# Performance work log

Hardware: AMD Instinct MI355X
Metric: run time of the kernel (lower is better)

Reference implementation:

```python
import jax, jax.numpy as jnp
import numpy as np

TOP_K = 2
HEAD_NUM = 16


def setup_inputs() -> dict:
    key = jax.random.key(0)
    ks = jax.random.split(key, 6)
    B, H, N, D, G = 8, HEAD_NUM, 2048, 64, 128
    return {
        "q": jax.random.normal(ks[0], (B, H, N, D), dtype=jnp.float32),
        "k": jax.random.normal(ks[1], (B, H, N, D), dtype=jnp.float32),
        "v": jax.random.normal(ks[2], (B, H, N, D), dtype=jnp.float32),
        "gating_input": jax.random.normal(ks[3], (B, N, G), dtype=jnp.float32),
        "rank3_ninf_mask": jnp.zeros((B, N, N), dtype=jnp.float32),
        "W_gate": jax.random.normal(ks[4], (H, G), dtype=jnp.float32) * 0.02,
        "b_gate": jnp.zeros((H,), dtype=jnp.float32),
    }


def reference(q, k, v, gating_input, rank3_ninf_mask, W_gate, b_gate):
    B = q.shape[0]
    d = q.shape[-1]
    # --- router ---
    gate_logits = gating_input.mean(axis=1) @ W_gate.T + b_gate      # [B, H]
    gate_softmax = jax.nn.softmax(gate_logits, axis=1)               # [B, H]
    _, top_k_idx = jax.lax.top_k(gate_softmax, TOP_K)                # [B, K]
    gating_mask = jnp.zeros_like(gate_softmax).at[
        jnp.arange(B)[:, None], top_k_idx].set(1.0)
    # load balancing loss
    tokens_per_expert = gating_mask.sum(axis=0)                      # [H]
    density = tokens_per_expert / (tokens_per_expert.sum() + 1e-6)
    lb_loss = HEAD_NUM * jnp.sum(gate_softmax.mean(axis=0) * density)
    # --- gather selected heads: [B, K, N, D] ---
    idx = top_k_idx[:, :, None, None]
    q_sel = jnp.take_along_axis(q, idx, axis=1)
    k_sel = jnp.take_along_axis(k, idx, axis=1)
    v_sel = jnp.take_along_axis(v, idx, axis=1)
    # --- scaled dot attention ---
    score = jnp.einsum('bhqd,bhkd->bhqk', q_sel, k_sel) / jnp.sqrt(
        jnp.asarray(d, dtype=q.dtype))                               # [B,K,N,N]
    score = score + rank3_ninf_mask[:, None, :, :]
    weights = jax.nn.softmax(score, axis=3)
    out = jnp.einsum('bhqk,bhkd->bhqd', weights, v_sel)              # [B,K,N,D]
    B_, K_, N_, D_ = out.shape
    out = out.transpose(0, 2, 1, 3).reshape(B_, N_, K_ * D_)         # [B,N,K*D]
    return out, lb_loss
```

## Files before the change

kernel.cpp:

```cpp
#include <hip/hip_runtime.h>

#define NSEQ 2048
#define DH 64
#define NH 16
#define BQ 64
#define BKV 64
#define KP 72
#define VP 68
#define PART_STRIDE 4224

typedef __attribute__((ext_vector_type(8))) short bf16x8;
typedef __attribute__((ext_vector_type(4))) short s16x4;
typedef __attribute__((ext_vector_type(4))) float f32x4;

static __device__ __forceinline__ short f2bf(float f) {
    __bf16 b = (__bf16)f;
    return __builtin_bit_cast(short, b);
}

__global__ void gate_partial(const float* __restrict__ gi, float* __restrict__ wsA, int SL) {
    int b = blockIdx.x / SL, sl = blockIdx.x % SL;
    int rows = NSEQ / SL;
    int tid = threadIdx.x;
    int g = tid & 127, half = tid >> 7;
    float s = 0.f;
    int n0 = sl * rows;
    for (int n = n0 + half; n < n0 + rows; n += 2)
        s += gi[((size_t)b * NSEQ + n) * 128 + g];
    __shared__ float part[2][128];
    part[half][g] = s;
    __syncthreads();
    if (tid < 128) wsA[(b * SL + sl) * 128 + tid] = part[0][tid] + part[1][tid];
}

__global__ void gate_final(const float* __restrict__ wsA, const float* __restrict__ Wg,
                           const float* __restrict__ bg, float* __restrict__ ws_sm,
                           int* __restrict__ ws_idx, int SL) {
    int b = blockIdx.x, tid = threadIdx.x;
    __shared__ float meanv[128];
    __shared__ float logits[NH];
    if (tid < 128) {
        float s = 0.f;
        for (int sl = 0; sl < SL; ++sl) s += wsA[(b * SL + sl) * 128 + tid];
        meanv[tid] = s * (1.0f / NSEQ);
    }
    __syncthreads();
    if (tid < 128) {
        int h = tid >> 3, j = tid & 7;
        float p = 0.f;
        for (int i = 0; i < 16; ++i) { int g = j + 8 * i; p += meanv[g] * Wg[h * 128 + g]; }
        p += __shfl_xor(p, 1);
        p += __shfl_xor(p, 2);
        p += __shfl_xor(p, 4);
        if (j == 0) logits[h] = p + bg[h];
    }
    __syncthreads();
    if (tid == 0) {
        float mx = logits[0];
        for (int h = 1; h < NH; ++h) mx = fmaxf(mx, logits[h]);
        float e[NH], sum = 0.f;
        for (int h = 0; h < NH; ++h) { e[h] = __expf(logits[h] - mx); sum += e[h]; }
        float inv = 1.0f / sum;
        for (int h = 0; h < NH; ++h) ws_sm[b * NH + h] = e[h] * inv;
        int i1 = 0;
        for (int h = 1; h < NH; ++h) if (logits[h] > logits[i1]) i1 = h;
        int i2 = (i1 == 0) ? 1 : 0;
        for (int h = 0; h < NH; ++h) if (h != i1 && logits[h] > logits[i2]) i2 = h;
        ws_idx[b * 2 + 0] = i1;
        ws_idx[b * 2 + 1] = i2;
    }
}

__global__ void lb_kernel(const float* __restrict__ ws_sm, const int* __restrict__ ws_idx,
                          float* __restrict__ out_lb) {
    if (threadIdx.x == 0 && blockIdx.x == 0) {
        float counts[NH];
        for (int h = 0; h < NH; ++h) counts[h] = 0.f;
        for (int i = 0; i < 16; ++i) counts[ws_idx[i]] += 1.0f;
        float lb = 0.f;
        for (int h = 0; h < NH; ++h) {
            float msm = 0.f;
            for (int b = 0; b < 8; ++b) msm += ws_sm[b * NH + h];
            msm *= (1.0f / 8.0f);
            lb += msm * (counts[h] / (16.0f + 1e-6f));
        }
        out_lb[0] = lb * (float)NH;
    }
}

template<int SPLIT>
__global__ __launch_bounds__(256, 4)
void attn_kernel(const float* __restrict__ q, const float* __restrict__ k,
                 const float* __restrict__ v, const float* __restrict__ mask,
                 const int* __restrict__ topk, float* __restrict__ out,
                 float* __restrict__ part) {
    const int qt = blockIdx.x & 31;
    const int sp = blockIdx.x >> 5;
    const int kk = blockIdx.y;
    const int b  = blockIdx.z;
    const int h  = topk[b * 2 + kk];
    const int tid = threadIdx.x;
    const int wave = tid >> 6;
    const int lane = tid & 63;
    const int lr = lane & 15;
    const int lg = lane >> 4;

    const int nt = 32 / SPLIT;
    const int t_begin = sp * nt;

    __shared__ short Kb[BKV][KP];
    __shared__ short Vt[DH][VP];
    __shared__ short Pl[4][16][VP];

    const float QSC = 0.125f * 1.4426950408889634f;
    const float MSC = 1.4426950408889634f;

    const size_t headoff = ((size_t)b * NH + h) * (size_t)NSEQ * DH;

    bf16x8 qf[2];
    {
        const float* qp = q + headoff + (size_t)(qt * BQ + wave * 16 + lr) * DH;
        #pragma unroll
        for (int f = 0; f < 2; ++f) {
            const float* p = qp + f * 32 + lg * 8;
            float4 a = *(const float4*)p;
            float4 c = *(const float4*)(p + 4);
            qf[f][0] = f2bf(a.x * QSC); qf[f][1] = f2bf(a.y * QSC);
            qf[f][2] = f2bf(a.z * QSC); qf[f][3] = f2bf(a.w * QSC);
            qf[f][4] = f2bf(c.x * QSC); qf[f][5] = f2bf(c.y * QSC);
            qf[f][6] = f2bf(c.z * QSC); qf[f][7] = f2bf(c.w * QSC);
        }
    }

    f32x4 acc[4];
    float m_r[4], l_r[4];
    #pragma unroll
    for (int dt = 0; dt < 4; ++dt)
        for (int r = 0; r < 4; ++r) acc[dt][r] = 0.f;
    #pragma unroll
    for (int r = 0; r < 4; ++r) { m_r[r] = -INFINITY; l_r[r] = 0.f; }

    const float* kb = k + headoff;
    const float* vb = v + headoff;
    const float* mb = mask + (size_t)b * NSEQ * NSEQ + (size_t)(qt * BQ + wave * 16) * NSEQ;

    const int srow = tid >> 4;
    const int scol = (tid & 15) * 4;

    float4 kreg[4], vreg[4];
    float  mreg[16];

    auto issue_kv = [&](int t0) {
        #pragma unroll
        for (int pp = 0; pp < 4; ++pp) {
            int n = t0 + pp * 16 + srow;
            kreg[pp] = *(const float4*)(kb + (size_t)n * DH + scol);
            vreg[pp] = *(const float4*)(vb + (size_t)n * DH + scol);
        }
    };
    auto issue_mask = [&](int t0) {
        #pragma unroll
        for (int r = 0; r < 4; ++r) {
            const float* mp = mb + (size_t)(4 * lg + r) * NSEQ + t0 + lr;
            #pragma unroll
            for (int ct = 0; ct < 4; ++ct) mreg[r * 4 + ct] = mp[ct * 16];
        }
    };

    issue_kv(t_begin * BKV);
    issue_mask(t_begin * BKV);

    for (int t = 0; t < nt; ++t) {
        const int t0 = (t_begin + t) * BKV;
        __syncthreads();
        #pragma unroll
        for (int pp = 0; pp < 4; ++pp) {
            int n = pp * 16 + srow;
            s16x4 sk = { f2bf(kreg[pp].x), f2bf(kreg[pp].y), f2bf(kreg[pp].z), f2bf(kreg[pp].w) };
            *(s16x4*)&Kb[n][scol] = sk;
            Vt[scol + 0][n] = f2bf(vreg[pp].x);
            Vt[scol + 1][n] = f2bf(vreg[pp].y);
            Vt[scol + 2][n] = f2bf(vreg[pp].z);
            Vt[scol + 3][n] = f2bf(vreg[pp].w);
        }
        __syncthreads();

        f32x4 s[4];
        #pragma unroll
        for (int ct = 0; ct < 4; ++ct) {
            bf16x8 kf0 = *(const bf16x8*)&Kb[ct * 16 + lr][lg * 8];
            bf16x8 kf1 = *(const bf16x8*)&Kb[ct * 16 + lr][32 + lg * 8];
            f32x4 z; for (int r = 0; r < 4; ++r) z[r] = 0.f;
            z = __builtin_amdgcn_mfma_f32_16x16x32_bf16(qf[0], kf0, z, 0, 0, 0);
            z = __builtin_amdgcn_mfma_f32_16x16x32_bf16(qf[1], kf1, z, 0, 0, 0);
            s[ct] = z;
        }
        #pragma unroll
        for (int r = 0; r < 4; ++r)
            #pragma unroll
            for (int ct = 0; ct < 4; ++ct)
                s[ct][r] = fmaf(mreg[r * 4 + ct], MSC, s[ct][r]);

        if (t + 1 < nt) { issue_kv(t0 + BKV); issue_mask(t0 + BKV); }

        float mnew[4], sc[4], ps[4];
        #pragma unroll
        for (int r = 0; r < 4; ++r) {
            float tm = fmaxf(fmaxf(s[0][r], s[1][r]), fmaxf(s[2][r], s[3][r]));
            tm = fmaxf(tm, __shfl_xor(tm, 1));
            tm = fmaxf(tm, __shfl_xor(tm, 2));
            tm = fmaxf(tm, __shfl_xor(tm, 4));
            tm = fmaxf(tm, __shfl_xor(tm, 8));
            mnew[r] = fmaxf(m_r[r], tm);
            sc[r] = __builtin_amdgcn_exp2f(m_r[r] - mnew[r]);
            ps[r] = 0.f;
        }
        #pragma unroll
        for (int ct = 0; ct < 4; ++ct) {
            #pragma unroll
            for (int r = 0; r < 4; ++r) {
                float p = __builtin_amdgcn_exp2f(s[ct][r] - mnew[r]);
                ps[r] += p;
                Pl[wave][4 * lg + r][ct * 16 + lr] = f2bf(p);
            }
        }
        #pragma unroll
        for (int r = 0; r < 4; ++r) {
            float t2 = ps[r];
            t2 += __shfl_xor(t2, 1);
            t2 += __shfl_xor(t2, 2);
            t2 += __shfl_xor(t2, 4);
            t2 += __shfl_xor(t2, 8);
            l_r[r] = l_r[r] * sc[r] + t2;
            m_r[r] = mnew[r];
        }
        #pragma unroll
        for (int dt = 0; dt < 4; ++dt)
            for (int r = 0; r < 4; ++r) acc[dt][r] *= sc[r];

        s16x4 p00 = *(const s16x4*)&Pl[wave][lr][lg * 8];
        s16x4 p01 = *(const s16x4*)&Pl[wave][lr][lg * 8 + 4];
        s16x4 p10 = *(const s16x4*)&Pl[wave][lr][32 + lg * 8];
        s16x4 p11 = *(const s16x4*)&Pl[wave][lr][32 + lg * 8 + 4];
        bf16x8 pf0 = __builtin_shufflevector(p00, p01, 0, 1, 2, 3, 4, 5, 6, 7);
        bf16x8 pf1 = __builtin_shufflevector(p10, p11, 0, 1, 2, 3, 4, 5, 6, 7);
        #pragma unroll
        for (int dt = 0; dt < 4; ++dt) {
            s16x4 v00 = *(const s16x4*)&Vt[dt * 16 + lr][lg * 8];
            s16x4 v01 = *(const s16x4*)&Vt[dt * 16 + lr][lg * 8 + 4];
            s16x4 v10 = *(const s16x4*)&Vt[dt * 16 + lr][32 + lg * 8];
            s16x4 v11 = *(const s16x4*)&Vt[dt * 16 + lr][32 + lg * 8 + 4];
            bf16x8 vf0 = __builtin_shufflevector(v00, v01, 0, 1, 2, 3, 4, 5, 6, 7);
            bf16x8 vf1 = __builtin_shufflevector(v10, v11, 0, 1, 2, 3, 4, 5, 6, 7);
            acc[dt] = __builtin_amdgcn_mfma_f32_16x16x32_bf16(pf0, vf0, acc[dt], 0, 0, 0);
            acc[dt] = __builtin_amdgcn_mfma_f32_16x16x32_bf16(pf1, vf1, acc[dt], 0, 0, 0);
        }
    }

    if (SPLIT == 1) {
        #pragma unroll
        for (int r = 0; r < 4; ++r) {
            float inv = 1.0f / l_r[r];
            int qrow = qt * BQ + wave * 16 + 4 * lg + r;
            float* op = out + ((size_t)b * NSEQ + qrow) * 128 + kk * 64;
            for (int dt = 0; dt < 4; ++dt) op[dt * 16 + lr] = acc[dt][r] * inv;
        }
    } else {
        float* pp = part + (size_t)((((b * 2 + kk) * 32 + qt) * SPLIT) + sp) * PART_STRIDE;
        #pragma unroll
        for (int r = 0; r < 4; ++r) {
            int prow = wave * 16 + 4 * lg + r;
            float* op = pp + prow * 64;
            for (int dt = 0; dt < 4; ++dt) op[dt * 16 + lr] = acc[dt][r];
            if (lr == 0) {
                pp[4096 + prow] = m_r[r];
                pp[4160 + prow] = l_r[r];
            }
        }
    }
}

__global__ __launch_bounds__(256)
void combine_kernel(const float* __restrict__ part, float* __restrict__ out, int SPLIT) {
    const int qt = blockIdx.x, kk = blockIdx.y, b = blockIdx.z;
    const float* base = part + (size_t)(((b * 2 + kk) * 32 + qt) * SPLIT) * PART_STRIDE;
    const int row = threadIdx.x >> 2;
    const int c0 = (threadIdx.x & 3) << 4;

    float M = -INFINITY;
    for (int s = 0; s < SPLIT; ++s)
        M = fmaxf(M, base[(size_t)s * PART_STRIDE + 4096 + row]);

    float L = 0.f;
    float4 o[4];
    #pragma unroll
    for (int j = 0; j < 4; ++j) o[j] = make_float4(0.f, 0.f, 0.f, 0.f);

    for (int s = 0; s < SPLIT; ++s) {
        const float* pb = base + (size_t)s * PART_STRIDE;
        float w = exp2f(pb[4096 + row] - M);
        L += w * pb[4160 + row];
        const float4* ap = (const float4*)(pb + row * 64 + c0);
        #pragma unroll
        for (int j = 0; j < 4; ++j) {
            float4 a = ap[j];
            o[j].x += w * a.x; o[j].y += w * a.y;
            o[j].z += w * a.z; o[j].w += w * a.w;
        }
    }
    float inv = 1.0f / L;
    float* op = out + ((size_t)b * NSEQ + qt * 64 + row) * 128 + kk * 64 + c0;
    #pragma unroll
    for (int j = 0; j < 4; ++j) {
        float4 r = make_float4(o[j].x * inv, o[j].y * inv, o[j].z * inv, o[j].w * inv);
        ((float4*)op)[j] = r;
    }
}

extern "C" void kernel_launch(void* const* d_in, const int* in_sizes, int n_in,
                              void* d_out, int out_size, void* d_ws, size_t ws_size,
                              hipStream_t stream) {
    const float* q    = (const float*)d_in[0];
    const float* k    = (const float*)d_in[1];
    const float* v    = (const float*)d_in[2];
    const float* gi   = (const float*)d_in[3];
    const float* mask = (const float*)d_in[4];
    const float* Wg   = (const float*)d_in[5];
    const float* bg   = (const float*)d_in[6];
    float* out = (float*)d_out;

    const size_t part_bytes = (size_t)512 * 4 * PART_STRIDE * 4;
    const size_t needA = part_bytes + (size_t)8 * 64 * 128 * 4 + 4096;
    const size_t needB = 65536 + part_bytes;

    int SL, SPLIT;
    float* ws_part;
    float* wsA;
    if (ws_size >= needA) {
        SL = 64; SPLIT = 4;
        ws_part = (float*)d_ws;
        wsA = (float*)((char*)d_ws + part_bytes);
    } else if (ws_size >= needB) {
        SL = 8; SPLIT = 4;
        wsA = (float*)d_ws;
        ws_part = (float*)((char*)d_ws + 65536);
    } else {
        SL = 8; SPLIT = 1;
        wsA = (float*)d_ws;
        ws_part = (float*)d_ws;
    }
    float* ws_sm = wsA + 8 * SL * 128;
    int*   ws_idx = (int*)(ws_sm + 8 * NH);

    gate_partial<<<8 * SL, 256, 0, stream>>>(gi, wsA, SL);
    gate_final<<<8, 256, 0, stream>>>(wsA, Wg, bg, ws_sm, ws_idx, SL);
    lb_kernel<<<1, 64, 0, stream>>>(ws_sm, ws_idx, out + (size_t)8 * NSEQ * 128);

    dim3 grid(32 * SPLIT, 2, 8);
    if (SPLIT == 4) {
        attn_kernel<4><<<grid, 256, 0, stream>>>(q, k, v, mask, ws_idx, out, ws_part);
        dim3 cgrid(32, 2, 8);
        combine_kernel<<<cgrid, 256, 0, stream>>>(ws_part, out, SPLIT);
    } else {
        attn_kernel<1><<<grid, 256, 0, stream>>>(q, k, v, mask, ws_idx, out, ws_part);
    }
}
```

Before: 114.9 us.

## Switch attention to 32x32x16 MFMA with 128-row query tiles and lazy rescale

Rewrites the attention kernel to use 32x32x16 bf16 MFMA with transposed S=K·Q^T, so each wave covers 32 query rows and a block covers 128. P fragments are built in registers through cross-half lane shuffles instead of a round trip through shared memory. Running-max rescaling is skipped unless the max grows past a threshold. K/V staging uses wider LDS stores, and the load-balance scalar is folded into the combine kernel so one launch is removed. The trade-offs are fewer blocks in the grid, a lower occupancy hint, and the thresholded rescale, which lets exp2 arguments reach up to the threshold (2^10) before renormalising.

New measurement: 117.7 us. +2.5%, slower.

```diff
diff --git a/kernel.cpp b/kernel.cpp
--- a/kernel.cpp
+++ b/kernel.cpp
@@ -3,15 +3,14 @@
 #define NSEQ 2048
 #define DH 64
 #define NH 16
-#define BQ 64
 #define BKV 64
-#define KP 72
-#define VP 68
-#define PART_STRIDE 4224
+#define PSTRIDE 8448
 
 typedef __attribute__((ext_vector_type(8))) short bf16x8;
 typedef __attribute__((ext_vector_type(4))) short s16x4;
 typedef __attribute__((ext_vector_type(4))) float f32x4;
+typedef __attribute__((ext_vector_type(16))) float f32x16;
+typedef __attribute__((ext_vector_type(4))) unsigned u32x4;
 
 static __device__ __forceinline__ short f2bf(float f) {
     __bf16 b = (__bf16)f;
@@ -71,100 +70,122 @@
     }
 }
 
+static __device__ __forceinline__ void lb_compute(const float* ws_sm, const int* ws_idx,
+                                                  float* out_lb) {
+    float counts[NH];
+    for (int h = 0; h < NH; ++h) counts[h] = 0.f;
+    for (int i = 0; i < 16; ++i) counts[ws_idx[i]] += 1.0f;
+    float lb = 0.f;
+    for (int h = 0; h < NH; ++h) {
+        float msm = 0.f;
+        for (int b = 0; b < 8; ++b) msm += ws_sm[b * NH + h];
+        msm *= (1.0f / 8.0f);
+        lb += msm * (counts[h] / (16.0f + 1e-6f));
+    }
+    out_lb[0] = lb * (float)NH;
+}
+
 __global__ void lb_kernel(const float* __restrict__ ws_sm, const int* __restrict__ ws_idx,
                           float* __restrict__ out_lb) {
-    if (threadIdx.x == 0 && blockIdx.x == 0) {
-        float counts[NH];
-        for (int h = 0; h < NH; ++h) counts[h] = 0.f;
-        for (int i = 0; i < 16; ++i) counts[ws_idx[i]] += 1.0f;
-        float lb = 0.f;
-        for (int h = 0; h < NH; ++h) {
-            float msm = 0.f;
-            for (int b = 0; b < 8; ++b) msm += ws_sm[b * NH + h];
-            msm *= (1.0f / 8.0f);
-            lb += msm * (counts[h] / (16.0f + 1e-6f));
-        }
-        out_lb[0] = lb * (float)NH;
-    }
+    if (threadIdx.x == 0 && blockIdx.x == 0) lb_compute(ws_sm, ws_idx, out_lb);
 }
 
 template<int SPLIT>
-__global__ __launch_bounds__(256, 4)
+__global__ __launch_bounds__(256, 3)
 void attn_kernel(const float* __restrict__ q, const float* __restrict__ k,
                  const float* __restrict__ v, const float* __restrict__ mask,
                  const int* __restrict__ topk, float* __restrict__ out,
                  float* __restrict__ part) {
-    const int qt = blockIdx.x & 31;
-    const int sp = blockIdx.x >> 5;
+    const int qt = blockIdx.x & 15;
+    const int sp = blockIdx.x >> 4;
     const int kk = blockIdx.y;
     const int b  = blockIdx.z;
-    const int h  = topk[b * 2 + kk];
+    const int hh = topk[b * 2 + kk];
     const int tid = threadIdx.x;
     const int wave = tid >> 6;
     const int lane = tid & 63;
-    const int lr = lane & 15;
-    const int lg = lane >> 4;
+    const int lq = lane & 31;
+    const int hi = lane >> 5;
 
     const int nt = 32 / SPLIT;
     const int t_begin = sp * nt;
 
-    __shared__ short Kb[BKV][KP];
-    __shared__ short Vt[DH][VP];
-    __shared__ short Pl[4][16][VP];
+    __shared__ short Kb[64][72];
+    __shared__ short Vt[64][72];
+    __shared__ float scb[4][32];
 
     const float QSC = 0.125f * 1.4426950408889634f;
     const float MSC = 1.4426950408889634f;
-
-    const size_t headoff = ((size_t)b * NH + h) * (size_t)NSEQ * DH;
-
-    bf16x8 qf[2];
+    const float THR = 10.0f;
+
+    const size_t headoff = ((size_t)b * NH + hh) * (size_t)NSEQ * DH;
+    const int qbase = qt * 128 + wave * 32;
+
+    bf16x8 qf[4];
     {
-        const float* qp = q + headoff + (size_t)(qt * BQ + wave * 16 + lr) * DH;
-        #pragma unroll
-        for (int f = 0; f < 2; ++f) {
-            const float* p = qp + f * 32 + lg * 8;
+        const float* qp = q + headoff + (size_t)(qbase + lq) * DH;
+        #pragma unroll
+        for (int dk = 0; dk < 4; ++dk) {
+            const float* p = qp + dk * 16 + hi * 8;
             float4 a = *(const float4*)p;
             float4 c = *(const float4*)(p + 4);
-            qf[f][0] = f2bf(a.x * QSC); qf[f][1] = f2bf(a.y * QSC);
-            qf[f][2] = f2bf(a.z * QSC); qf[f][3] = f2bf(a.w * QSC);
-            qf[f][4] = f2bf(c.x * QSC); qf[f][5] = f2bf(c.y * QSC);
-            qf[f][6] = f2bf(c.z * QSC); qf[f][7] = f2bf(c.w * QSC);
-        }
-    }
-
-    f32x4 acc[4];
-    float m_r[4], l_r[4];
+            bf16x8 f = { f2bf(a.x * QSC), f2bf(a.y * QSC), f2bf(a.z * QSC), f2bf(a.w * QSC),
+                         f2bf(c.x * QSC), f2bf(c.y * QSC), f2bf(c.z * QSC), f2bf(c.w * QSC) };
+            qf[dk] = f;
+        }
+    }
+
+    f32x16 acc0, acc1;
     #pragma unroll
-    for (int dt = 0; dt < 4; ++dt)
-        for (int r = 0; r < 4; ++r) acc[dt][r] = 0.f;
-    #pragma unroll
-    for (int r = 0; r < 4; ++r) { m_r[r] = -INFINITY; l_r[r] = 0.f; }
+    for (int r = 0; r < 16; ++r) { acc0[r] = 0.f; acc1[r] = 0.f; }
+    float m_r = -1e30f, l_r = 0.f;
 
     const float* kb = k + headoff;
     const float* vb = v + headoff;
-    const float* mb = mask + (size_t)b * NSEQ * NSEQ + (size_t)(qt * BQ + wave * 16) * NSEQ;
-
-    const int srow = tid >> 4;
-    const int scol = (tid & 15) * 4;
-
-    float4 kreg[4], vreg[4];
-    float  mreg[16];
+    const float* mb = mask + (size_t)b * NSEQ * NSEQ + (size_t)(qbase + lq) * NSEQ;
+
+    const int krow = tid >> 3;
+    const int kcol = (tid & 7) * 8;
+    const int vrow = (tid & 15) * 4;
+    const int vcol = (tid >> 4) * 4;
+
+    float4 kreg[4], vreg[4], mreg[8];
 
     auto issue_kv = [&](int t0) {
-        #pragma unroll
-        for (int pp = 0; pp < 4; ++pp) {
-            int n = t0 + pp * 16 + srow;
-            kreg[pp] = *(const float4*)(kb + (size_t)n * DH + scol);
-            vreg[pp] = *(const float4*)(vb + (size_t)n * DH + scol);
-        }
+        const float* kp = kb + (size_t)(t0 + krow) * DH + kcol;
+        kreg[0] = *(const float4*)kp;
+        kreg[1] = *(const float4*)(kp + 4);
+        kreg[2] = *(const float4*)(kp + 32 * DH);
+        kreg[3] = *(const float4*)(kp + 32 * DH + 4);
+        const float* vp = vb + (size_t)(t0 + vrow) * DH + vcol;
+        #pragma unroll
+        for (int i = 0; i < 4; ++i) vreg[i] = *(const float4*)(vp + i * DH);
     };
     auto issue_mask = [&](int t0) {
-        #pragma unroll
-        for (int r = 0; r < 4; ++r) {
-            const float* mp = mb + (size_t)(4 * lg + r) * NSEQ + t0 + lr;
-            #pragma unroll
-            for (int ct = 0; ct < 4; ++ct) mreg[r * 4 + ct] = mp[ct * 16];
-        }
+        const float* mp = mb + t0 + hi * 4;
+        #pragma unroll
+        for (int g = 0; g < 4; ++g) {
+            mreg[g]     = *(const float4*)(mp + g * 8);
+            mreg[4 + g] = *(const float4*)(mp + 32 + g * 8);
+        }
+    };
+
+    auto pack2 = [&](float a, float bb) -> unsigned {
+        union { short s[2]; unsigned u; } t;
+        t.s[0] = f2bf(a); t.s[1] = f2bf(bb);
+        return t.u;
+    };
+    auto buildfrag = [&](float a0, float a1, float a2, float a3,
+                         float a4, float a5, float a6, float a7) -> bf16x8 {
+        unsigned pk01 = pack2(a0, a1), pk23 = pack2(a2, a3);
+        unsigned pk45 = pack2(a4, a5), pk67 = pack2(a6, a7);
+        unsigned ta = hi ? pk01 : pk45;
+        unsigned tb = hi ? pk23 : pk67;
+        unsigned ya = __shfl_xor(ta, 32);
+        unsigned yb = __shfl_xor(tb, 32);
+        u32x4 fr = { hi ? ya : pk01, hi ? yb : pk23,
+                     hi ? pk45 : ya, hi ? pk67 : yb };
+        return __builtin_bit_cast(bf16x8, fr);
     };
 
     issue_kv(t_begin * BKV);
@@ -173,148 +194,169 @@
     for (int t = 0; t < nt; ++t) {
         const int t0 = (t_begin + t) * BKV;
         __syncthreads();
-        #pragma unroll
-        for (int pp = 0; pp < 4; ++pp) {
-            int n = pp * 16 + srow;
-            s16x4 sk = { f2bf(kreg[pp].x), f2bf(kreg[pp].y), f2bf(kreg[pp].z), f2bf(kreg[pp].w) };
-            *(s16x4*)&Kb[n][scol] = sk;
-            Vt[scol + 0][n] = f2bf(vreg[pp].x);
-            Vt[scol + 1][n] = f2bf(vreg[pp].y);
-            Vt[scol + 2][n] = f2bf(vreg[pp].z);
-            Vt[scol + 3][n] = f2bf(vreg[pp].w);
+        {
+            bf16x8 k0 = { f2bf(kreg[0].x), f2bf(kreg[0].y), f2bf(kreg[0].z), f2bf(kreg[0].w),
+                          f2bf(kreg[1].x), f2bf(kreg[1].y), f2bf(kreg[1].z), f2bf(kreg[1].w) };
+            bf16x8 k1 = { f2bf(kreg[2].x), f2bf(kreg[2].y), f2bf(kreg[2].z), f2bf(kreg[2].w),
+                          f2bf(kreg[3].x), f2bf(kreg[3].y), f2bf(kreg[3].z), f2bf(kreg[3].w) };
+            *(bf16x8*)&Kb[krow][kcol] = k0;
+            *(bf16x8*)&Kb[krow + 32][kcol] = k1;
+            s16x4 c0v = { f2bf(vreg[0].x), f2bf(vreg[1].x), f2bf(vreg[2].x), f2bf(vreg[3].x) };
+            s16x4 c1v = { f2bf(vreg[0].y), f2bf(vreg[1].y), f2bf(vreg[2].y), f2bf(vreg[3].y) };
+            s16x4 c2v = { f2bf(vreg[0].z), f2bf(vreg[1].z), f2bf(vreg[2].z), f2bf(vreg[3].z) };
+            s16x4 c3v = { f2bf(vreg[0].w), f2bf(vreg[1].w), f2bf(vreg[2].w), f2bf(vreg[3].w) };
+            *(s16x4*)&Vt[vcol + 0][vrow] = c0v;
+            *(s16x4*)&Vt[vcol + 1][vrow] = c1v;
+            *(s16x4*)&Vt[vcol + 2][vrow] = c2v;
+            *(s16x4*)&Vt[vcol + 3][vrow] = c3v;
         }
         __syncthreads();
 
-        f32x4 s[4];
-        #pragma unroll
-        for (int ct = 0; ct < 4; ++ct) {
-            bf16x8 kf0 = *(const bf16x8*)&Kb[ct * 16 + lr][lg * 8];
-            bf16x8 kf1 = *(const bf16x8*)&Kb[ct * 16 + lr][32 + lg * 8];
-            f32x4 z; for (int r = 0; r < 4; ++r) z[r] = 0.f;
-            z = __builtin_amdgcn_mfma_f32_16x16x32_bf16(qf[0], kf0, z, 0, 0, 0);
-            z = __builtin_amdgcn_mfma_f32_16x16x32_bf16(qf[1], kf1, z, 0, 0, 0);
-            s[ct] = z;
-        }
-        #pragma unroll
-        for (int r = 0; r < 4; ++r)
+        f32x16 S0, S1;
+        #pragma unroll
+        for (int r = 0; r < 16; ++r) { S0[r] = 0.f; S1[r] = 0.f; }
+        #pragma unroll
+        for (int dk = 0; dk < 4; ++dk) {
+            bf16x8 kf0 = *(const bf16x8*)&Kb[lq][dk * 16 + hi * 8];
+            bf16x8 kf1 = *(const bf16x8*)&Kb[32 + lq][dk * 16 + hi * 8];
+            S0 = __builtin_amdgcn_mfma_f32_32x32x16_bf16(kf0, qf[dk], S0, 0, 0, 0);
+            S1 = __builtin_amdgcn_mfma_f32_32x32x16_bf16(kf1, qf[dk], S1, 0, 0, 0);
+        }
+        #pragma unroll
+        for (int g = 0; g < 4; ++g) {
+            S0[4*g+0] = fmaf(mreg[g].x, MSC, S0[4*g+0]);
+            S0[4*g+1] = fmaf(mreg[g].y, MSC, S0[4*g+1]);
+            S0[4*g+2] = fmaf(mreg[g].z, MSC, S0[4*g+2]);
+            S0[4*g+3] = fmaf(mreg[g].w, MSC, S0[4*g+3]);
+            S1[4*g+0] = fmaf(mreg[4+g].x, MSC, S1[4*g+0]);
+            S1[4*g+1] = fmaf(mreg[4+g].y, MSC, S1[4*g+1]);
+            S1[4*g+2] = fmaf(mreg[4+g].z, MSC, S1[4*g+2]);
+            S1[4*g+3] = fmaf(mreg[4+g].w, MSC, S1[4*g+3]);
+        }
+
+        if (t + 1 < nt) issue_kv(t0 + BKV);
+
+        float tmx[16];
+        #pragma unroll
+        for (int r = 0; r < 16; ++r) tmx[r] = fmaxf(S0[r], S1[r]);
+        #pragma unroll
+        for (int w2 = 8; w2 > 0; w2 >>= 1)
             #pragma unroll
-            for (int ct = 0; ct < 4; ++ct)
-                s[ct][r] = fmaf(mreg[r * 4 + ct], MSC, s[ct][r]);
-
-        if (t + 1 < nt) { issue_kv(t0 + BKV); issue_mask(t0 + BKV); }
-
-        float mnew[4], sc[4], ps[4];
-        #pragma unroll
-        for (int r = 0; r < 4; ++r) {
-            float tm = fmaxf(fmaxf(s[0][r], s[1][r]), fmaxf(s[2][r], s[3][r]));
-            tm = fmaxf(tm, __shfl_xor(tm, 1));
-            tm = fmaxf(tm, __shfl_xor(tm, 2));
-            tm = fmaxf(tm, __shfl_xor(tm, 4));
-            tm = fmaxf(tm, __shfl_xor(tm, 8));
-            mnew[r] = fmaxf(m_r[r], tm);
-            sc[r] = __builtin_amdgcn_exp2f(m_r[r] - mnew[r]);
-            ps[r] = 0.f;
-        }
-        #pragma unroll
-        for (int ct = 0; ct < 4; ++ct) {
+            for (int r = 0; r < 8; ++r) if (r < w2) tmx[r] = fmaxf(tmx[r], tmx[r + w2]);
+        float pm = fmaxf(tmx[0], __shfl_xor(tmx[0], 32));
+
+        if (__any(pm > m_r + THR)) {
+            float mnew = fmaxf(m_r, pm);
+            float scw = __builtin_amdgcn_exp2f(m_r - mnew);
+            if (lane < 32) scb[wave][lane] = scw;
             #pragma unroll
-            for (int r = 0; r < 4; ++r) {
-                float p = __builtin_amdgcn_exp2f(s[ct][r] - mnew[r]);
-                ps[r] += p;
-                Pl[wave][4 * lg + r][ct * 16 + lr] = f2bf(p);
+            for (int g = 0; g < 4; ++g) {
+                float4 s4 = *(const float4*)&scb[wave][hi * 4 + g * 8];
+                acc0[4*g+0] *= s4.x; acc1[4*g+0] *= s4.x;
+                acc0[4*g+1] *= s4.y; acc1[4*g+1] *= s4.y;
+                acc0[4*g+2] *= s4.z; acc1[4*g+2] *= s4.z;
+                acc0[4*g+3] *= s4.w; acc1[4*g+3] *= s4.w;
             }
-        }
-        #pragma unroll
-        for (int r = 0; r < 4; ++r) {
-            float t2 = ps[r];
-            t2 += __shfl_xor(t2, 1);
-            t2 += __shfl_xor(t2, 2);
-            t2 += __shfl_xor(t2, 4);
-            t2 += __shfl_xor(t2, 8);
-            l_r[r] = l_r[r] * sc[r] + t2;
-            m_r[r] = mnew[r];
-        }
-        #pragma unroll
-        for (int dt = 0; dt < 4; ++dt)
-            for (int r = 0; r < 4; ++r) acc[dt][r] *= sc[r];
-
-        s16x4 p00 = *(const s16x4*)&Pl[wave][lr][lg * 8];
-        s16x4 p01 = *(const s16x4*)&Pl[wave][lr][lg * 8 + 4];
-        s16x4 p10 = *(const s16x4*)&Pl[wave][lr][32 + lg * 8];
-        s16x4 p11 = *(const s16x4*)&Pl[wave][lr][32 + lg * 8 + 4];
-        bf16x8 pf0 = __builtin_shufflevector(p00, p01, 0, 1, 2, 3, 4, 5, 6, 7);
-        bf16x8 pf1 = __builtin_shufflevector(p10, p11, 0, 1, 2, 3, 4, 5, 6, 7);
-        #pragma unroll
-        for (int dt = 0; dt < 4; ++dt) {
-            s16x4 v00 = *(const s16x4*)&Vt[dt * 16 + lr][lg * 8];
-            s16x4 v01 = *(const s16x4*)&Vt[dt * 16 + lr][lg * 8 + 4];
-            s16x4 v10 = *(const s16x4*)&Vt[dt * 16 + lr][32 + lg * 8];
-            s16x4 v11 = *(const s16x4*)&Vt[dt * 16 + lr][32 + lg * 8 + 4];
-            bf16x8 vf0 = __builtin_shufflevector(v00, v01, 0, 1, 2, 3, 4, 5, 6, 7);
-            bf16x8 vf1 = __builtin_shufflevector(v10, v11, 0, 1, 2, 3, 4, 5, 6, 7);
-            acc[dt] = __builtin_amdgcn_mfma_f32_16x16x32_bf16(pf0, vf0, acc[dt], 0, 0, 0);
-            acc[dt] = __builtin_amdgcn_mfma_f32_16x16x32_bf16(pf1, vf1, acc[dt], 0, 0, 0);
+            l_r *= scw; m_r = mnew;
+        }
+        float ps = 0.f;
+        #pragma unroll
+        for (int r = 0; r < 16; ++r) { float p = __builtin_amdgcn_exp2f(S0[r] - m_r); ps += p; S0[r] = p; }
+        #pragma unroll
+        for (int r = 0; r < 16; ++r) { float p = __builtin_amdgcn_exp2f(S1[r] - m_r); ps += p; S1[r] = p; }
+        ps += __shfl_xor(ps, 32);
+        l_r += ps;
+
+        bf16x8 pf0 = buildfrag(S0[0], S0[1], S0[2],  S0[3],  S0[4],  S0[5],  S0[6],  S0[7]);
+        bf16x8 pf1 = buildfrag(S0[8], S0[9], S0[10], S0[11], S0[12], S0[13], S0[14], S0[15]);
+        bf16x8 pf2 = buildfrag(S1[0], S1[1], S1[2],  S1[3],  S1[4],  S1[5],  S1[6],  S1[7]);
+        bf16x8 pf3 = buildfrag(S1[8], S1[9], S1[10], S1[11], S1[12], S1[13], S1[14], S1[15]);
+
+        if (t + 1 < nt) issue_mask(t0 + BKV);
+
+        #pragma unroll
+        for (int c = 0; c < 4; ++c) {
+            bf16x8 pf = (c == 0) ? pf0 : (c == 1) ? pf1 : (c == 2) ? pf2 : pf3;
+            bf16x8 vf0 = *(const bf16x8*)&Vt[lq][c * 16 + hi * 8];
+            bf16x8 vf1 = *(const bf16x8*)&Vt[32 + lq][c * 16 + hi * 8];
+            acc0 = __builtin_amdgcn_mfma_f32_32x32x16_bf16(pf, vf0, acc0, 0, 0, 0);
+            acc1 = __builtin_amdgcn_mfma_f32_32x32x16_bf16(pf, vf1, acc1, 0, 0, 0);
         }
     }
 
     if (SPLIT == 1) {
-        #pragma unroll
-        for (int r = 0; r < 4; ++r) {
-            float inv = 1.0f / l_r[r];
-            int qrow = qt * BQ + wave * 16 + 4 * lg + r;
-            float* op = out + ((size_t)b * NSEQ + qrow) * 128 + kk * 64;
-            for (int dt = 0; dt < 4; ++dt) op[dt * 16 + lr] = acc[dt][r] * inv;
+        if (lane < 32) scb[wave][lane] = 1.0f / l_r;
+        #pragma unroll
+        for (int g = 0; g < 4; ++g) {
+            float4 s4 = *(const float4*)&scb[wave][hi * 4 + g * 8];
+            #pragma unroll
+            for (int j = 0; j < 4; ++j) {
+                int qrow = qbase + hi * 4 + g * 8 + j;
+                float sc = (j == 0) ? s4.x : (j == 1) ? s4.y : (j == 2) ? s4.z : s4.w;
+                float* op = out + ((size_t)b * NSEQ + qrow) * 128 + kk * 64;
+                op[lq]      = acc0[4*g+j] * sc;
+                op[32 + lq] = acc1[4*g+j] * sc;
+            }
         }
     } else {
-        float* pp = part + (size_t)((((b * 2 + kk) * 32 + qt) * SPLIT) + sp) * PART_STRIDE;
-        #pragma unroll
-        for (int r = 0; r < 4; ++r) {
-            int prow = wave * 16 + 4 * lg + r;
-            float* op = pp + prow * 64;
-            for (int dt = 0; dt < 4; ++dt) op[dt * 16 + lr] = acc[dt][r];
-            if (lr == 0) {
-                pp[4096 + prow] = m_r[r];
-                pp[4160 + prow] = l_r[r];
+        float* pp = part + (size_t)((((b * 2 + kk) * 16 + qt) * SPLIT) + sp) * PSTRIDE;
+        #pragma unroll
+        for (int g = 0; g < 4; ++g) {
+            #pragma unroll
+            for (int j = 0; j < 4; ++j) {
+                int qloc = wave * 32 + hi * 4 + g * 8 + j;
+                pp[qloc * 64 + lq]      = acc0[4*g+j];
+                pp[qloc * 64 + 32 + lq] = acc1[4*g+j];
             }
         }
+        if (lane < 32) {
+            int wl = wave * 32 + lane;
+            pp[8192 + wl] = m_r;
+            pp[8320 + wl] = l_r;
+        }
     }
 }
 
 __global__ __launch_bounds__(256)
-void combine_kernel(const float* __restrict__ part, float* __restrict__ out, int SPLIT) {
+void combine_kernel(const float* __restrict__ part, float* __restrict__ out,
+                    const float* __restrict__ ws_sm, const int* __restrict__ ws_idx,
+                    float* __restrict__ out_lb) {
     const int qt = blockIdx.x, kk = blockIdx.y, b = blockIdx.z;
-    const float* base = part + (size_t)(((b * 2 + kk) * 32 + qt) * SPLIT) * PART_STRIDE;
-    const int row = threadIdx.x >> 2;
-    const int c0 = (threadIdx.x & 3) << 4;
-
-    float M = -INFINITY;
-    for (int s = 0; s < SPLIT; ++s)
-        M = fmaxf(M, base[(size_t)s * PART_STRIDE + 4096 + row]);
+    const float* base = part + (size_t)(((b * 2 + kk) * 16 + qt) * 4) * PSTRIDE;
+    const int row = threadIdx.x >> 1;
+    const int half = threadIdx.x & 1;
+
+    float M = -1e30f;
+    #pragma unroll
+    for (int s = 0; s < 4; ++s) M = fmaxf(M, base[(size_t)s * PSTRIDE + 8192 + row]);
 
     float L = 0.f;
-    float4 o[4];
+    float4 o[8];
     #pragma unroll
-    for (int j = 0; j < 4; ++j) o[j] = make_float4(0.f, 0.f, 0.f, 0.f);
-
-    for (int s = 0; s < SPLIT; ++s) {
-        const float* pb = base + (size_t)s * PART_STRIDE;
-        float w = exp2f(pb[4096 + row] - M);
-        L += w * pb[4160 + row];
-        const float4* ap = (const float4*)(pb + row * 64 + c0);
-        #pragma unroll
-        for (int j = 0; j < 4; ++j) {
+    for (int j = 0; j < 8; ++j) o[j] = make_float4(0.f, 0.f, 0.f, 0.f);
+
+    #pragma unroll
+    for (int s = 0; s < 4; ++s) {
+        const float* pb = base + (size_t)s * PSTRIDE;
+        float w = __builtin_amdgcn_exp2f(pb[8192 + row] - M);
+        L += w * pb[8320 + row];
+        const float4* ap = (const float4*)(pb + row * 64 + half * 32);
+        #pragma unroll
+        for (int j = 0; j < 8; ++j) {
             float4 a = ap[j];
             o[j].x += w * a.x; o[j].y += w * a.y;
             o[j].z += w * a.z; o[j].w += w * a.w;
         }
     }
     float inv = 1.0f / L;
-    float* op = out + ((size_t)b * NSEQ + qt * 64 + row) * 128 + kk * 64 + c0;
+    float* op = out + ((size_t)b * NSEQ + qt * 128 + row) * 128 + kk * 64 + half * 32;
     #pragma unroll
-    for (int j = 0; j < 4; ++j) {
+    for (int j = 0; j < 8; ++j) {
         float4 r = make_float4(o[j].x * inv, o[j].y * inv, o[j].z * inv, o[j].w * inv);
         ((float4*)op)[j] = r;
     }
+    if (qt == 0 && kk == 0 && b == 0 && threadIdx.x == 0)
+        lb_compute(ws_sm, ws_idx, out_lb);
 }
 
 extern "C" void kernel_launch(void* const* d_in, const int* in_sizes, int n_in,
@@ -328,9 +370,11 @@
     const float* Wg   = (const float*)d_in[5];
     const float* bg   = (const float*)d_in[6];
     float* out = (float*)d_out;
-
-    const size_t part_bytes = (size_t)512 * 4 * PART_STRIDE * 4;
-    const size_t needA = part_bytes + (size_t)8 * 64 * 128 * 4 + 4096;
+    float* out_lb = out + (size_t)8 * NSEQ * 128;
+
+    const size_t part_bytes = (size_t)1024 * PSTRIDE * 4;
+    const size_t gateA_bytes = (size_t)8 * 64 * 128 * 4 + 4096;
+    const size_t needA = part_bytes + gateA_bytes;
     const size_t needB = 65536 + part_bytes;
 
     int SL, SPLIT;
@@ -354,14 +398,15 @@
 
     gate_partial<<<8 * SL, 256, 0, stream>>>(gi, wsA, SL);
     gate_final<<<8, 256, 0, stream>>>(wsA, Wg, bg, ws_sm, ws_idx, SL);
-    lb_kernel<<<1, 64, 0, stream>>>(ws_sm, ws_idx, out + (size_t)8 * NSEQ * 128);
-
-    dim3 grid(32 * SPLIT, 2, 8);
+
     if (SPLIT == 4) {
+        dim3 grid(16 * 4, 2, 8);
         attn_kernel<4><<<grid, 256, 0, stream>>>(q, k, v, mask, ws_idx, out, ws_part);
-        dim3 cgrid(32, 2, 8);
-        combine_kernel<<<cgrid, 256, 0, stream>>>(ws_part, out, SPLIT);
+        dim3 cgrid(16, 2, 8);
+        combine_kernel<<<cgrid, 256, 0, stream>>>(ws_part, out, ws_sm, ws_idx, out_lb);
     } else {
+        lb_kernel<<<1, 64, 0, stream>>>(ws_sm, ws_idx, out_lb);
+        dim3 grid(16, 2, 8);
         attn_kernel<1><<<grid, 256, 0, stream>>>(q, k, v, mask, ws_idx, out, ws_part);
     }
 }
```
